# Kernel optimization log

Measured on AMD Instinct MI355X. Metric: run time of the kernel, lower is better.

The kernel has to match this reference:

```python
import jax, jax.numpy as jnp
import numpy as np

DIM = 1024
ATT_DIM = 1024
NUM_HEADS = 16
HEAD_DIM = ATT_DIM // NUM_HEADS


def setup_inputs() -> dict:
    key = jax.random.key(0)
    ks = jax.random.split(key, 13)
    s = lambda fan_in: 1.0 / np.sqrt(fan_in)
    bsz, n = 8, 1024
    x = jax.random.normal(ks[0], (bsz, n, DIM), dtype=jnp.float32)
    # Linear weights stored as [in, out] (apply via x @ W + b)
    Wq = jax.random.uniform(ks[1], (DIM, ATT_DIM), minval=-s(DIM), maxval=s(DIM))
    bq = jax.random.uniform(ks[2], (ATT_DIM,), minval=-s(DIM), maxval=s(DIM))
    Wk = jax.random.uniform(ks[3], (DIM, ATT_DIM), minval=-s(DIM), maxval=s(DIM))
    bk = jax.random.uniform(ks[4], (ATT_DIM,), minval=-s(DIM), maxval=s(DIM))
    Wv = jax.random.uniform(ks[5], (DIM, ATT_DIM), minval=-s(DIM), maxval=s(DIM))
    bv = jax.random.uniform(ks[6], (ATT_DIM,), minval=-s(DIM), maxval=s(DIM))
    Win = jax.random.uniform(ks[7], (DIM, HEAD_DIM), minval=-s(DIM), maxval=s(DIM))
    bin_ = jax.random.uniform(ks[8], (HEAD_DIM,), minval=-s(DIM), maxval=s(DIM))
    d_in1 = HEAD_DIM * (NUM_HEADS + 1)
    W1 = jax.random.uniform(ks[9], (d_in1, 2 * DIM), minval=-s(d_in1), maxval=s(d_in1))
    b1 = jax.random.uniform(ks[10], (2 * DIM,), minval=-s(d_in1), maxval=s(d_in1))
    W2 = jax.random.uniform(ks[11], (2 * DIM, DIM), minval=-s(2 * DIM), maxval=s(2 * DIM))
    b2 = jax.random.uniform(ks[12], (DIM,), minval=-s(2 * DIM), maxval=s(2 * DIM))
    return {"x": x, "Wq": Wq, "bq": bq, "Wk": Wk, "bk": bk, "Wv": Wv, "bv": bv,
            "Win": Win, "bin_": bin_, "W1": W1, "b1": b1, "W2": W2, "b2": b2}


def reference(x, Wq, bq, Wk, bk, Wv, bv, Win, bin_, W1, b1, W2, b2):
    bsz, n, _ = x.shape
    scaling = HEAD_DIM ** (-0.5)
    # [b, n, h, d]
    q = (x @ Wq + bq).reshape(bsz, n, NUM_HEADS, HEAD_DIM) * scaling
    k = (x @ Wk + bk).reshape(bsz, n, NUM_HEADS, HEAD_DIM)
    v = (x @ Wv + bv).reshape(bsz, n, NUM_HEADS, HEAD_DIM)
    # scores [b, h, n, n]
    score = jnp.einsum('bihd,bjhd->bhij', q, k)
    diag = jnp.eye(n, dtype=bool)  # self positions masked with -inf
    score = jnp.where(diag[None, None], -jnp.inf, score)
    attn = jax.nn.softmax(score, axis=-1)
    out = jnp.einsum('bhij,bjhd->bihd', attn, v).reshape(bsz, n, NUM_HEADS * HEAD_DIM)
    in_ = (x @ Win + bin_)  # [b, n, head_dim]
    out = jnp.concatenate([out, in_], axis=-1)
    h = jax.nn.relu(out @ W1 + b1)
    return h @ W2 + b2
```

## Files before the change

### kernel.cpp

```cpp
#include <hip/hip_runtime.h>

typedef __bf16 bf16;
typedef __attribute__((ext_vector_type(8))) __bf16 bf16x8;
typedef __attribute__((ext_vector_type(4))) __bf16 bf16x4;
typedef __attribute__((ext_vector_type(4))) short short4_t;
typedef __attribute__((ext_vector_type(4))) float floatx4;

typedef const void __attribute__((address_space(1)))* gas1p;
typedef void __attribute__((address_space(3)))* las3p;

#define LOG2E 1.44269504088896340736f

static constexpr int D_MODEL = 1024;
static constexpr int N_HEADS = 16;
static constexpr int HDIM    = 64;
static constexpr int BSZ     = 8;
static constexpr int SEQ     = 1024;
static constexpr int ROWS    = BSZ * SEQ;
static constexpr int FF_IN   = 1088;
static constexpr int FF_HID  = 2048;
static constexpr int QKV_LD  = 3072;

__device__ __forceinline__ floatx4 mfma_bf16(bf16x8 a, bf16x8 b, floatx4 c) {
  return __builtin_amdgcn_mfma_f32_16x16x32_bf16(a, b, c, 0, 0, 0);
}

__device__ __forceinline__ floatx4 mfma16(bf16x4 a, bf16x4 b, floatx4 c) {
#if __has_builtin(__builtin_amdgcn_mfma_f32_16x16x16_bf16)
  return __builtin_amdgcn_mfma_f32_16x16x16_bf16(a, b, c, 0, 0, 0);
#else
  return __builtin_amdgcn_mfma_f32_16x16x16bf16_1k(
      __builtin_bit_cast(short4_t, a), __builtin_bit_cast(short4_t, b), c, 0, 0, 0);
#endif
}

__device__ __forceinline__ float flex_load(const void* src, size_t idx, int isbf) {
  return isbf ? (float)((const bf16*)src)[idx] : ((const float*)src)[idx];
}

__global__ void detect_kernel(const unsigned* __restrict__ w, int* __restrict__ flag) {
  __shared__ int cnt;
  if (threadIdx.x == 0) cnt = 0;
  __syncthreads();
  int hits = 0;
  for (int i = threadIdx.x; i < 4096; i += 256) {
    const unsigned v = w[(size_t)i * 997 + 13];
    const unsigned b = (v >> 8) & 0x7F;
    hits += (b >= 0x3B && b <= 0x41) ? 1 : 0;
  }
  atomicAdd(&cnt, hits);
  __syncthreads();
  if (threadIdx.x == 0) *flag = (cnt > 2048) ? 1 : 0;
}

__global__ __launch_bounds__(256)
void x_to_bf16_kernel(const void* __restrict__ src, bf16* __restrict__ dst,
                      const int* __restrict__ flag) {
  const int isbf = *flag;
  const size_t i = ((size_t)blockIdx.x * 256 + threadIdx.x) * 8;
  bf16x8 o;
  if (isbf) {
    o = *reinterpret_cast<const bf16x8*>((const bf16*)src + i);
  } else {
    const float4 f0 = *reinterpret_cast<const float4*>((const float*)src + i);
    const float4 f1 = *reinterpret_cast<const float4*>((const float*)src + i + 4);
    o[0] = (bf16)f0.x; o[1] = (bf16)f0.y; o[2] = (bf16)f0.z; o[3] = (bf16)f0.w;
    o[4] = (bf16)f1.x; o[5] = (bf16)f1.y; o[6] = (bf16)f1.z; o[7] = (bf16)f1.w;
  }
  *reinterpret_cast<bf16x8*>(dst + i) = o;
}

__global__ __launch_bounds__(256)
void bias_all_kernel(const void* bq, const void* bk, const void* bv,
                     const void* bin, const void* b1, const void* b2,
                     float* __restrict__ dst, const int* __restrict__ flag) {
  const int isbf = *flag;
  const int i = blockIdx.x * 256 + threadIdx.x;
  if (i < 1024)      dst[i] = flex_load(bq, i, isbf) * 0.125f;
  else if (i < 2048) dst[i] = flex_load(bk, i - 1024, isbf);
  else if (i < 3072) dst[i] = flex_load(bv, i - 2048, isbf);
  else if (i < 3136) dst[i] = flex_load(bin, i - 3072, isbf);
  else if (i < 5184) dst[i] = flex_load(b1, i - 3136, isbf);
  else if (i < 6208) dst[i] = flex_load(b2, i - 5184, isbf);
}

struct TransJobs {
  const void* src[6];
  bf16* dst[6];
  int R[6], C[6];
  int tiles_x[6];
  int tile_base[7];
  float scale[6];
};

__global__ __launch_bounds__(256)
void transpose_all_kernel(TransJobs J, const int* __restrict__ flag) {
  __shared__ float tile[32][33];
  const int isbf = *flag;
  const int bid = blockIdx.x;
  int j = 0;
#pragma unroll
  for (int t = 1; t < 6; t++) j += (bid >= J.tile_base[t]) ? 1 : 0;
  const int t = bid - J.tile_base[j];
  const int c0 = (t % J.tiles_x[j]) * 32, r0 = (t / J.tiles_x[j]) * 32;
  const void* src = J.src[j];
  bf16* dst = J.dst[j];
  const int R = J.R[j], C = J.C[j];
  const float scale = J.scale[j];
  const int tx = threadIdx.x & 31, ty = threadIdx.x >> 5;
  for (int i = ty; i < 32; i += 8)
    tile[i][tx] = flex_load(src, (size_t)(r0 + i) * C + (c0 + tx), isbf);
  __syncthreads();
  for (int i = ty; i < 32; i += 8)
    dst[(size_t)(c0 + i) * R + (r0 + tx)] = (bf16)(tile[tx][i] * scale);
}

__global__ __launch_bounds__(256)
void transpose_v_kernel(const bf16* __restrict__ v, bf16* __restrict__ vt) {
  __shared__ float tile[32][33];
  const int bh = blockIdx.z, b = bh >> 4, h = bh & 15;
  const int s0 = blockIdx.x * 32, d0 = blockIdx.y * 32;
  const int tx = threadIdx.x & 31, ty = threadIdx.x >> 5;
  const bf16* src = v + (size_t)b * SEQ * QKV_LD + 2048 + h * HDIM;
  bf16* dst = vt + (size_t)bh * HDIM * SEQ;
  for (int i = ty; i < 32; i += 8)
    tile[i][tx] = (float)src[(size_t)(s0 + i) * QKV_LD + d0 + tx];
  __syncthreads();
  for (int i = ty; i < 32; i += 8)
    dst[(size_t)(d0 + i) * SEQ + s0 + tx] = (bf16)tile[tx][i];
}

template <int BN, bool DO_RELU, bool OUT_FLEX>
__global__ __launch_bounds__(256)
void gemm_bt(const bf16* __restrict__ A, const bf16* __restrict__ BT,
             const float* __restrict__ bias,
             void* __restrict__ Cv, int N, int K, int ldc,
             bf16* __restrict__ C2, int ldc2, int nsplit, int nvalid,
             const int* __restrict__ flag) {
  constexpr int BM = 128, BK = 64;
  constexpr int TCN = BN / 32;
  constexpr int ACH = (BM * BK) / (256 * 8);
  constexpr int BCH = (BN * BK) / (256 * 8);
  __shared__ bf16 As[BM * BK];
  __shared__ bf16 Bs[BN * BK];
  const int tid = threadIdx.x;
  const int wave = tid >> 6, lane = tid & 63;
  const int quad = lane >> 4, lo = lane & 15;
  const int wm = wave >> 1, wn = wave & 1;
  const int m0 = blockIdx.x * BM;
  const int n0 = blockIdx.y * BN;

  floatx4 acc[4][TCN];
#pragma unroll
  for (int i = 0; i < 4; i++)
#pragma unroll
    for (int j = 0; j < TCN; j++) acc[i][j] = floatx4{0.f, 0.f, 0.f, 0.f};

  for (int kb = 0; kb < K; kb += BK) {
#pragma unroll
    for (int u = 0; u < ACH; u++) {
      const int c = u * 256 + tid;
      const int row = c >> 3, col = c & 7;
      const int gcol = col ^ (row & 7);
      const bf16* g = A + (size_t)(m0 + row) * K + kb + gcol * 8;
      __builtin_amdgcn_global_load_lds((gas1p)g, (las3p)(As + c * 8), 16, 0, 0);
    }
#pragma unroll
    for (int u = 0; u < BCH; u++) {
      const int c = u * 256 + tid;
      const int row = c >> 3, col = c & 7;
      const int gcol = col ^ (row & 7);
      const bf16* g = BT + (size_t)(n0 + row) * K + kb + gcol * 8;
      __builtin_amdgcn_global_load_lds((gas1p)g, (las3p)(Bs + c * 8), 16, 0, 0);
    }
    __syncthreads();
#pragma unroll
    for (int kk = 0; kk < 2; kk++) {
      bf16x8 af[4], bfr[TCN];
#pragma unroll
      for (int tr = 0; tr < 4; tr++) {
        const int row = wm * 64 + tr * 16 + lo;
        const int cc = (kk * 4 + quad) ^ (lo & 7);
        af[tr] = *reinterpret_cast<const bf16x8*>(As + row * BK + cc * 8);
      }
#pragma unroll
      for (int tc = 0; tc < TCN; tc++) {
        const int row = wn * (BN / 2) + tc * 16 + lo;
        const int cc = (kk * 4 + quad) ^ (lo & 7);
        bfr[tc] = *reinterpret_cast<const bf16x8*>(Bs + row * BK + cc * 8);
      }
#pragma unroll
      for (int tr = 0; tr < 4; tr++)
#pragma unroll
        for (int tc = 0; tc < TCN; tc++)
          acc[tr][tc] = mfma_bf16(af[tr], bfr[tc], acc[tr][tc]);
    }
    __syncthreads();
  }

  const int isbf = OUT_FLEX ? *flag : 1;
#pragma unroll
  for (int tc = 0; tc < TCN; tc++) {
    const int col = n0 + wn * (BN / 2) + tc * 16 + lo;
    const float bval = bias[col];
    if (col < nsplit) {
#pragma unroll
      for (int tr = 0; tr < 4; tr++) {
        const int rbase = m0 + wm * 64 + tr * 16 + quad * 4;
#pragma unroll
        for (int r = 0; r < 4; r++) {
          float v = acc[tr][tc][r] + bval;
          if (DO_RELU) v = fmaxf(v, 0.f);
          const size_t idx = (size_t)(rbase + r) * ldc + col;
          if (!OUT_FLEX || isbf) ((bf16*)Cv)[idx] = (bf16)v;
          else                   ((float*)Cv)[idx] = v;
        }
      }
    } else if (col < nvalid) {
#pragma unroll
      for (int tr = 0; tr < 4; tr++) {
        const int rbase = m0 + wm * 64 + tr * 16 + quad * 4;
#pragma unroll
        for (int r = 0; r < 4; r++) {
          float v = acc[tr][tc][r] + bval;
          if (DO_RELU) v = fmaxf(v, 0.f);
          C2[(size_t)(rbase + r) * ldc2 + (col - nsplit)] = (bf16)v;
        }
      }
    }
  }
}

__global__ __launch_bounds__(256)
void attn_kernel(const bf16* __restrict__ QKV, const bf16* __restrict__ Vt,
                 bf16* __restrict__ Cc) {
  __shared__ bf16 Ks[64 * 64];
  __shared__ bf16 Vs[64 * 64];
  const int bid = blockIdx.x;
  const int xcd = bid & 7, g = bid >> 3;
  const int ib = g & 7, bh = (g >> 3) * 8 + xcd;
  const int b = bh >> 4, h = bh & 15;
  const int i0 = ib * 128;
  const int tid = threadIdx.x, wave = tid >> 6, lane = tid & 63;
  const int quad = lane >> 4, lo = lane & 15;
  const int iw = i0 + wave * 32;
  const bf16* qptr = QKV + (size_t)b * SEQ * QKV_LD + h * HDIM;
  const bf16* kptr = QKV + (size_t)b * SEQ * QKV_LD + 1024 + h * HDIM;
  const bf16* vptr = Vt + (size_t)bh * HDIM * SEQ;

  bf16x8 qf[2][2];
#pragma unroll
  for (int it = 0; it < 2; it++)
#pragma unroll
    for (int kf = 0; kf < 2; kf++)
      qf[it][kf] = *reinterpret_cast<const bf16x8*>(
          qptr + (size_t)(iw + it * 16 + lo) * QKV_LD + kf * 32 + quad * 8);

  floatx4 oacc[2][4];
  float lrow[2] = {0.f, 0.f};
#pragma unroll
  for (int it = 0; it < 2; it++)
#pragma unroll
    for (int dt = 0; dt < 4; dt++) oacc[it][dt] = floatx4{0.f, 0.f, 0.f, 0.f};

  for (int jb = 0; jb < SEQ / 64; jb++) {
    const int j0 = jb * 64;
#pragma unroll
    for (int u = 0; u < 2; u++) {
      const int c = u * 256 + tid;
      const int row = c >> 3, col = c & 7;
      const int gcol = col ^ (row & 7);
      __builtin_amdgcn_global_load_lds(
          (gas1p)(kptr + (size_t)(j0 + row) * QKV_LD + gcol * 8),
          (las3p)(Ks + c * 8), 16, 0, 0);
      __builtin_amdgcn_global_load_lds(
          (gas1p)(vptr + (size_t)row * SEQ + j0 + gcol * 8),
          (las3p)(Vs + c * 8), 16, 0, 0);
    }
    __syncthreads();

    floatx4 sacc[2][4];
#pragma unroll
    for (int it = 0; it < 2; it++)
#pragma unroll
      for (int mt = 0; mt < 4; mt++) sacc[it][mt] = floatx4{0.f, 0.f, 0.f, 0.f};
#pragma unroll
    for (int mt = 0; mt < 4; mt++) {
      const int r = mt * 16 + lo;
      const int cc0 = quad ^ (lo & 7);
      const int cc1 = (4 + quad) ^ (lo & 7);
      const bf16x8 k0 = *reinterpret_cast<const bf16x8*>(Ks + r * 64 + cc0 * 8);
      const bf16x8 k1 = *reinterpret_cast<const bf16x8*>(Ks + r * 64 + cc1 * 8);
#pragma unroll
      for (int it = 0; it < 2; it++) {
        sacc[it][mt] = mfma_bf16(k0, qf[it][0], sacc[it][mt]);
        sacc[it][mt] = mfma_bf16(k1, qf[it][1], sacc[it][mt]);
      }
    }

    if (j0 == (iw & ~63)) {
#pragma unroll
      for (int it = 0; it < 2; it++) {
        const int ig = iw + it * 16 + lo;
#pragma unroll
        for (int mt = 0; mt < 4; mt++)
#pragma unroll
          for (int r = 0; r < 4; r++)
            if (j0 + mt * 16 + quad * 4 + r == ig) sacc[it][mt][r] = -1e30f;
      }
    }

    bf16x4 pfrag[2][4];
#pragma unroll
    for (int it = 0; it < 2; it++) {
      float s = 0.f;
#pragma unroll
      for (int mt = 0; mt < 4; mt++) {
        bf16x4 pk;
#pragma unroll
        for (int r = 0; r < 4; r++) {
          const float p = exp2f(sacc[it][mt][r] * LOG2E);
          s += p;
          pk[r] = (bf16)p;
        }
        pfrag[it][mt] = pk;
      }
      s += __shfl_xor(s, 16);
      s += __shfl_xor(s, 32);
      lrow[it] += s;
    }

#pragma unroll
    for (int dt = 0; dt < 4; dt++) {
      const int r = dt * 16 + lo;
#pragma unroll
      for (int kt = 0; kt < 4; kt++) {
        const int gch = kt * 2 + (quad >> 1);
        const int cc = gch ^ (lo & 7);
        const bf16x4 vf = *reinterpret_cast<const bf16x4*>(
            Vs + r * 64 + cc * 8 + (quad & 1) * 4);
#pragma unroll
        for (int it = 0; it < 2; it++)
          oacc[it][dt] = mfma16(vf, pfrag[it][kt], oacc[it][dt]);
      }
    }
    __syncthreads();
  }

#pragma unroll
  for (int it = 0; it < 2; it++) {
    const int ig = iw + it * 16 + lo;
    const float inv = 1.0f / lrow[it];
    bf16* cb = Cc + ((size_t)b * SEQ + ig) * FF_IN + h * HDIM;
#pragma unroll
    for (int dt = 0; dt < 4; dt++) {
      bf16x4 o;
#pragma unroll
      for (int r = 0; r < 4; r++) o[r] = (bf16)(oacc[it][dt][r] * inv);
      *reinterpret_cast<bf16x4*>(cb + dt * 16 + quad * 4) = o;
    }
  }
}

extern "C" void kernel_launch(void* const* d_in, const int* in_sizes, int n_in,
                              void* d_out, int out_size, void* d_ws, size_t ws_size,
                              hipStream_t stream) {
  (void)in_sizes; (void)n_in; (void)out_size; (void)ws_size;
  const void* x   = d_in[0];
  const void* Wq  = d_in[1];
  const void* bq  = d_in[2];
  const void* Wk  = d_in[3];
  const void* bk  = d_in[4];
  const void* Wv  = d_in[5];
  const void* bv  = d_in[6];
  const void* Win = d_in[7];
  const void* bin = d_in[8];
  const void* W1  = d_in[9];
  const void* b1  = d_in[10];
  const void* W2  = d_in[11];
  const void* b2  = d_in[12];

  size_t off = 0;
  char* wsb = (char*)d_ws;
  auto alloc = [&](size_t bytes) {
    void* p = (void*)(wsb + off);
    off += (bytes + 255) & ~(size_t)255;
    return p;
  };
  int*   flag  = (int*)alloc(4);
  bf16*  xbf   = (bf16*)alloc((size_t)ROWS * D_MODEL * 2);
  bf16*  WqkvT = (bf16*)alloc((size_t)3200 * 1024 * 2);
  bf16*  W1T   = (bf16*)alloc((size_t)FF_HID * FF_IN * 2);
  bf16*  W2T   = (bf16*)alloc((size_t)D_MODEL * FF_HID * 2);
  float* biasf = (float*)alloc(6208 * 4);
  bf16*  qkv   = (bf16*)alloc((size_t)ROWS * QKV_LD * 2);
  bf16*  vtb   = (bf16*)alloc((size_t)ROWS * D_MODEL * 2);
  bf16*  cbuf  = (bf16*)alloc((size_t)ROWS * FF_IN * 2);
  bf16*  hbuf  = (bf16*)alloc((size_t)ROWS * FF_HID * 2);
  float* b1f   = biasf + 3136;
  float* b2f   = biasf + 5184;

  const dim3 blk(256);
  detect_kernel<<<1, blk, 0, stream>>>((const unsigned*)x, flag);

  x_to_bf16_kernel<<<(ROWS * D_MODEL) / 2048, blk, 0, stream>>>(x, xbf, flag);
  bias_all_kernel<<<25, blk, 0, stream>>>(bq, bk, bv, bin, b1, b2, biasf, flag);

  TransJobs J;
  J.src[0] = Wq;  J.dst[0] = WqkvT;                        J.R[0] = 1024; J.C[0] = 1024; J.scale[0] = 0.125f;
  J.src[1] = Wk;  J.dst[1] = WqkvT + (size_t)1024 * 1024;  J.R[1] = 1024; J.C[1] = 1024; J.scale[1] = 1.0f;
  J.src[2] = Wv;  J.dst[2] = WqkvT + (size_t)2048 * 1024;  J.R[2] = 1024; J.C[2] = 1024; J.scale[2] = 1.0f;
  J.src[3] = Win; J.dst[3] = WqkvT + (size_t)3072 * 1024;  J.R[3] = 1024; J.C[3] = 64;   J.scale[3] = 1.0f;
  J.src[4] = W1;  J.dst[4] = W1T;                          J.R[4] = 1088; J.C[4] = 2048; J.scale[4] = 1.0f;
  J.src[5] = W2;  J.dst[5] = W2T;                          J.R[5] = 2048; J.C[5] = 1024; J.scale[5] = 1.0f;
  int base = 0;
  for (int j = 0; j < 6; j++) {
    J.tiles_x[j] = J.C[j] / 32;
    J.tile_base[j] = base;
    base += (J.R[j] / 32) * (J.C[j] / 32);
  }
  J.tile_base[6] = base;
  transpose_all_kernel<<<base, blk, 0, stream>>>(J, flag);

  gemm_bt<128, false, false><<<dim3(ROWS / 128, 25), blk, 0, stream>>>(
      xbf, WqkvT, biasf, qkv, 3200, 1024, QKV_LD,
      cbuf + 1024, FF_IN, 3072, 3136, nullptr);

  transpose_v_kernel<<<dim3(SEQ / 32, HDIM / 32, BSZ * N_HEADS), blk, 0, stream>>>(qkv, vtb);

  attn_kernel<<<dim3(1024), blk, 0, stream>>>(qkv, vtb, cbuf);

  gemm_bt<128, true, false><<<dim3(ROWS / 128, FF_HID / 128), blk, 0, stream>>>(
      cbuf, W1T, b1f, hbuf, FF_HID, FF_IN, FF_HID,
      nullptr, 0, FF_HID, FF_HID, nullptr);
  gemm_bt<128, false, true><<<dim3(ROWS / 128, D_MODEL / 128), blk, 0, stream>>>(
      hbuf, W2T, b2f, d_out, D_MODEL, FF_HID, D_MODEL,
      nullptr, 0, D_MODEL, D_MODEL, flag);
}
```

Baseline: 398.3 us.

## Double-buffer K/V tiles in attention and fold log2e into Q scaling

The attention kernel now keeps two LDS buffers for K and V and issues the next tile's global-to-LDS loads before computing on the current one, so load latency overlaps MFMA work. It also folds the log2e factor into the Q weight and bias scaling, which removes a multiply per score before exp2, splits the row-sum into two accumulators, and raises wave priority around the MFMA blocks. The cost is doubled LDS per block (32KB), which may reduce occupancy, and the correctness of the loop depends on the single barrier per iteration also covering the prefetch.

Result: slower. 407.6 us (+2.3%).

```diff
diff --git a/kernel.cpp b/kernel.cpp
--- a/kernel.cpp
+++ b/kernel.cpp
@@ -76,7 +76,7 @@
                      float* __restrict__ dst, const int* __restrict__ flag) {
   const int isbf = *flag;
   const int i = blockIdx.x * 256 + threadIdx.x;
-  if (i < 1024)      dst[i] = flex_load(bq, i, isbf) * 0.125f;
+  if (i < 1024)      dst[i] = flex_load(bq, i, isbf) * (0.125f * LOG2E);
   else if (i < 2048) dst[i] = flex_load(bk, i - 1024, isbf);
   else if (i < 3072) dst[i] = flex_load(bv, i - 2048, isbf);
   else if (i < 3136) dst[i] = flex_load(bin, i - 3072, isbf);
@@ -234,8 +234,8 @@
 __global__ __launch_bounds__(256)
 void attn_kernel(const bf16* __restrict__ QKV, const bf16* __restrict__ Vt,
                  bf16* __restrict__ Cc) {
-  __shared__ bf16 Ks[64 * 64];
-  __shared__ bf16 Vs[64 * 64];
+  __shared__ bf16 Ks[2][64 * 64];
+  __shared__ bf16 Vs[2][64 * 64];
   const int bid = blockIdx.x;
   const int xcd = bid & 7, g = bid >> 3;
   const int ib = g & 7, bh = (g >> 3) * 8 + xcd;
@@ -248,6 +248,10 @@
   const bf16* kptr = QKV + (size_t)b * SEQ * QKV_LD + 1024 + h * HDIM;
   const bf16* vptr = Vt + (size_t)bh * HDIM * SEQ;
 
+  const int c0 = tid, c1 = 256 + tid;
+  const int row0 = c0 >> 3, gcol0 = (c0 & 7) ^ (row0 & 7);
+  const int row1 = c1 >> 3, gcol1 = (c1 & 7) ^ (row1 & 7);
+
   bf16x8 qf[2][2];
 #pragma unroll
   for (int it = 0; it < 2; it++)
@@ -263,40 +267,65 @@
 #pragma unroll
     for (int dt = 0; dt < 4; dt++) oacc[it][dt] = floatx4{0.f, 0.f, 0.f, 0.f};
 
+  {
+    __builtin_amdgcn_global_load_lds(
+        (gas1p)(kptr + (size_t)row0 * QKV_LD + gcol0 * 8),
+        (las3p)(Ks[0] + c0 * 8), 16, 0, 0);
+    __builtin_amdgcn_global_load_lds(
+        (gas1p)(vptr + (size_t)row0 * SEQ + gcol0 * 8),
+        (las3p)(Vs[0] + c0 * 8), 16, 0, 0);
+    __builtin_amdgcn_global_load_lds(
+        (gas1p)(kptr + (size_t)row1 * QKV_LD + gcol1 * 8),
+        (las3p)(Ks[0] + c1 * 8), 16, 0, 0);
+    __builtin_amdgcn_global_load_lds(
+        (gas1p)(vptr + (size_t)row1 * SEQ + gcol1 * 8),
+        (las3p)(Vs[0] + c1 * 8), 16, 0, 0);
+  }
+  __syncthreads();
+
   for (int jb = 0; jb < SEQ / 64; jb++) {
     const int j0 = jb * 64;
-#pragma unroll
-    for (int u = 0; u < 2; u++) {
-      const int c = u * 256 + tid;
-      const int row = c >> 3, col = c & 7;
-      const int gcol = col ^ (row & 7);
+    const int cur = jb & 1;
+
+    if (jb + 1 < SEQ / 64) {
+      const int jn = j0 + 64;
       __builtin_amdgcn_global_load_lds(
-          (gas1p)(kptr + (size_t)(j0 + row) * QKV_LD + gcol * 8),
-          (las3p)(Ks + c * 8), 16, 0, 0);
+          (gas1p)(kptr + (size_t)(jn + row0) * QKV_LD + gcol0 * 8),
+          (las3p)(Ks[cur ^ 1] + c0 * 8), 16, 0, 0);
       __builtin_amdgcn_global_load_lds(
-          (gas1p)(vptr + (size_t)row * SEQ + j0 + gcol * 8),
-          (las3p)(Vs + c * 8), 16, 0, 0);
-    }
-    __syncthreads();
+          (gas1p)(vptr + (size_t)row0 * SEQ + jn + gcol0 * 8),
+          (las3p)(Vs[cur ^ 1] + c0 * 8), 16, 0, 0);
+      __builtin_amdgcn_global_load_lds(
+          (gas1p)(kptr + (size_t)(jn + row1) * QKV_LD + gcol1 * 8),
+          (las3p)(Ks[cur ^ 1] + c1 * 8), 16, 0, 0);
+      __builtin_amdgcn_global_load_lds(
+          (gas1p)(vptr + (size_t)row1 * SEQ + jn + gcol1 * 8),
+          (las3p)(Vs[cur ^ 1] + c1 * 8), 16, 0, 0);
+    }
+
+    const bf16* Kc = Ks[cur];
+    const bf16* Vc = Vs[cur];
 
     floatx4 sacc[2][4];
 #pragma unroll
     for (int it = 0; it < 2; it++)
 #pragma unroll
       for (int mt = 0; mt < 4; mt++) sacc[it][mt] = floatx4{0.f, 0.f, 0.f, 0.f};
+    __builtin_amdgcn_s_setprio(1);
 #pragma unroll
     for (int mt = 0; mt < 4; mt++) {
       const int r = mt * 16 + lo;
       const int cc0 = quad ^ (lo & 7);
       const int cc1 = (4 + quad) ^ (lo & 7);
-      const bf16x8 k0 = *reinterpret_cast<const bf16x8*>(Ks + r * 64 + cc0 * 8);
-      const bf16x8 k1 = *reinterpret_cast<const bf16x8*>(Ks + r * 64 + cc1 * 8);
+      const bf16x8 k0 = *reinterpret_cast<const bf16x8*>(Kc + r * 64 + cc0 * 8);
+      const bf16x8 k1 = *reinterpret_cast<const bf16x8*>(Kc + r * 64 + cc1 * 8);
 #pragma unroll
       for (int it = 0; it < 2; it++) {
         sacc[it][mt] = mfma_bf16(k0, qf[it][0], sacc[it][mt]);
         sacc[it][mt] = mfma_bf16(k1, qf[it][1], sacc[it][mt]);
       }
     }
+    __builtin_amdgcn_s_setprio(0);
 
     if (j0 == (iw & ~63)) {
 #pragma unroll
@@ -313,23 +342,25 @@
     bf16x4 pfrag[2][4];
 #pragma unroll
     for (int it = 0; it < 2; it++) {
-      float s = 0.f;
+      float s0 = 0.f, s1 = 0.f;
 #pragma unroll
       for (int mt = 0; mt < 4; mt++) {
         bf16x4 pk;
 #pragma unroll
         for (int r = 0; r < 4; r++) {
-          const float p = exp2f(sacc[it][mt][r] * LOG2E);
-          s += p;
+          const float p = exp2f(sacc[it][mt][r]);
+          if (mt & 1) s1 += p; else s0 += p;
           pk[r] = (bf16)p;
         }
         pfrag[it][mt] = pk;
       }
+      float s = s0 + s1;
       s += __shfl_xor(s, 16);
       s += __shfl_xor(s, 32);
       lrow[it] += s;
     }
 
+    __builtin_amdgcn_s_setprio(1);
 #pragma unroll
     for (int dt = 0; dt < 4; dt++) {
       const int r = dt * 16 + lo;
@@ -338,12 +369,14 @@
         const int gch = kt * 2 + (quad >> 1);
         const int cc = gch ^ (lo & 7);
         const bf16x4 vf = *reinterpret_cast<const bf16x4*>(
-            Vs + r * 64 + cc * 8 + (quad & 1) * 4);
+            Vc + r * 64 + cc * 8 + (quad & 1) * 4);
 #pragma unroll
         for (int it = 0; it < 2; it++)
           oacc[it][dt] = mfma16(vf, pfrag[it][kt], oacc[it][dt]);
       }
     }
+    __builtin_amdgcn_s_setprio(0);
+
     __syncthreads();
   }
 
@@ -407,7 +440,7 @@
   bias_all_kernel<<<25, blk, 0, stream>>>(bq, bk, bv, bin, b1, b2, biasf, flag);
 
   TransJobs J;
-  J.src[0] = Wq;  J.dst[0] = WqkvT;                        J.R[0] = 1024; J.C[0] = 1024; J.scale[0] = 0.125f;
+  J.src[0] = Wq;  J.dst[0] = WqkvT;                        J.R[0] = 1024; J.C[0] = 1024; J.scale[0] = 0.125f * LOG2E;
   J.src[1] = Wk;  J.dst[1] = WqkvT + (size_t)1024 * 1024;  J.R[1] = 1024; J.C[1] = 1024; J.scale[1] = 1.0f;
   J.src[2] = Wv;  J.dst[2] = WqkvT + (size_t)2048 * 1024;  J.R[2] = 1024; J.C[2] = 1024; J.scale[2] = 1.0f;
   J.src[3] = Win; J.dst[3] = WqkvT + (size_t)3072 * 1024;  J.R[3] = 1024; J.C[3] = 64;   J.scale[3] = 1.0f;
```

## Triple-buffer GEMM with 256x128 tiles, fold log2e into Q scaling

Applied to the files above, without the earlier changes.

The GEMM grows to 256x128 tiles run by 512 threads, with a three-stage LDS ring buffer. Async global-to-LDS loads are issued up to three K-steps ahead and tracked with explicit vmcnt waits, which hides global latency behind MFMA work. The attention kernel drops a multiply per score by folding LOG2E into the Q weight and bias scale, raises wave priority around its MFMA sections, and splits the row-sum accumulator in two. The ring buffer uses about 144KB of LDS per block, so only one block fits per CU despite the launch-bounds hint, and the larger tiles halve the grid size.

Measured after the change: 416.7 us. +4.6%, slower.

```diff
diff --git a/kernel.cpp b/kernel.cpp
--- a/kernel.cpp
+++ b/kernel.cpp
@@ -76,7 +76,7 @@
                      float* __restrict__ dst, const int* __restrict__ flag) {
   const int isbf = *flag;
   const int i = blockIdx.x * 256 + threadIdx.x;
-  if (i < 1024)      dst[i] = flex_load(bq, i, isbf) * 0.125f;
+  if (i < 1024)      dst[i] = flex_load(bq, i, isbf) * (0.125f * LOG2E);
   else if (i < 2048) dst[i] = flex_load(bk, i - 1024, isbf);
   else if (i < 3072) dst[i] = flex_load(bv, i - 2048, isbf);
   else if (i < 3136) dst[i] = flex_load(bin, i - 3072, isbf);
@@ -131,24 +131,24 @@
 }
 
 template <int BN, bool DO_RELU, bool OUT_FLEX>
-__global__ __launch_bounds__(256)
+__global__ __launch_bounds__(512, 2)
 void gemm_bt(const bf16* __restrict__ A, const bf16* __restrict__ BT,
              const float* __restrict__ bias,
              void* __restrict__ Cv, int N, int K, int ldc,
              bf16* __restrict__ C2, int ldc2, int nsplit, int nvalid,
              const int* __restrict__ flag) {
-  constexpr int BM = 128, BK = 64;
+  constexpr int BM = 256, BK = 64;
   constexpr int TCN = BN / 32;
-  constexpr int ACH = (BM * BK) / (256 * 8);
-  constexpr int BCH = (BN * BK) / (256 * 8);
-  __shared__ bf16 As[BM * BK];
-  __shared__ bf16 Bs[BN * BK];
+  static_assert(BN == 128, "BN must be 128");
+  __shared__ bf16 As[3][BM * BK];
+  __shared__ bf16 Bs[3][BN * BK];
   const int tid = threadIdx.x;
   const int wave = tid >> 6, lane = tid & 63;
   const int quad = lane >> 4, lo = lane & 15;
   const int wm = wave >> 1, wn = wave & 1;
   const int m0 = blockIdx.x * BM;
   const int n0 = blockIdx.y * BN;
+  const int NT = K / BK;
 
   floatx4 acc[4][TCN];
 #pragma unroll
@@ -156,24 +156,36 @@
 #pragma unroll
     for (int j = 0; j < TCN; j++) acc[i][j] = floatx4{0.f, 0.f, 0.f, 0.f};
 
-  for (int kb = 0; kb < K; kb += BK) {
-#pragma unroll
-    for (int u = 0; u < ACH; u++) {
-      const int c = u * 256 + tid;
-      const int row = c >> 3, col = c & 7;
-      const int gcol = col ^ (row & 7);
-      const bf16* g = A + (size_t)(m0 + row) * K + kb + gcol * 8;
-      __builtin_amdgcn_global_load_lds((gas1p)g, (las3p)(As + c * 8), 16, 0, 0);
-    }
-#pragma unroll
-    for (int u = 0; u < BCH; u++) {
-      const int c = u * 256 + tid;
-      const int row = c >> 3, col = c & 7;
-      const int gcol = col ^ (row & 7);
-      const bf16* g = BT + (size_t)(n0 + row) * K + kb + gcol * 8;
-      __builtin_amdgcn_global_load_lds((gas1p)g, (las3p)(Bs + c * 8), 16, 0, 0);
-    }
-    __syncthreads();
+  auto stage = [&](int t, int cb) {
+    const size_t kb = (size_t)t * BK;
+#pragma unroll
+    for (int u = 0; u < 4; u++) {
+      const int c = u * 512 + tid;
+      const int row = c >> 3;
+      const int gcol = (c & 7) ^ (row & 7);
+      __builtin_amdgcn_global_load_lds(
+          (gas1p)(A + (size_t)(m0 + row) * K + kb + gcol * 8),
+          (las3p)(&As[cb][c * 8]), 16, 0, 0);
+    }
+#pragma unroll
+    for (int u = 0; u < 2; u++) {
+      const int c = u * 512 + tid;
+      const int row = c >> 3;
+      const int gcol = (c & 7) ^ (row & 7);
+      __builtin_amdgcn_global_load_lds(
+          (gas1p)(BT + (size_t)(n0 + row) * K + kb + gcol * 8),
+          (las3p)(&Bs[cb][c * 8]), 16, 0, 0);
+    }
+  };
+
+  stage(0, 0); stage(1, 1); stage(2, 2);
+  asm volatile("s_waitcnt vmcnt(12)" ::: "memory");
+  asm volatile("s_barrier" ::: "memory");
+
+  for (int kt = 0; kt < NT; ++kt) {
+    const int cb = kt % 3;
+    const bf16* Asc = As[cb];
+    const bf16* Bsc = Bs[cb];
 #pragma unroll
     for (int kk = 0; kk < 2; kk++) {
       bf16x8 af[4], bfr[TCN];
@@ -181,13 +193,13 @@
       for (int tr = 0; tr < 4; tr++) {
         const int row = wm * 64 + tr * 16 + lo;
         const int cc = (kk * 4 + quad) ^ (lo & 7);
-        af[tr] = *reinterpret_cast<const bf16x8*>(As + row * BK + cc * 8);
+        af[tr] = *reinterpret_cast<const bf16x8*>(Asc + row * BK + cc * 8);
       }
 #pragma unroll
       for (int tc = 0; tc < TCN; tc++) {
         const int row = wn * (BN / 2) + tc * 16 + lo;
         const int cc = (kk * 4 + quad) ^ (lo & 7);
-        bfr[tc] = *reinterpret_cast<const bf16x8*>(Bs + row * BK + cc * 8);
+        bfr[tc] = *reinterpret_cast<const bf16x8*>(Bsc + row * BK + cc * 8);
       }
 #pragma unroll
       for (int tr = 0; tr < 4; tr++)
@@ -195,7 +207,16 @@
         for (int tc = 0; tc < TCN; tc++)
           acc[tr][tc] = mfma_bf16(af[tr], bfr[tc], acc[tr][tc]);
     }
-    __syncthreads();
+    if (kt + 1 < NT) {
+      asm volatile("s_waitcnt lgkmcnt(0)" ::: "memory");
+      asm volatile("s_barrier" ::: "memory");
+      if (kt + 3 < NT) stage(kt + 3, cb);
+      const int ahead = ((kt + 3 < NT) ? (kt + 3) : (NT - 1)) - (kt + 1);
+      if (ahead >= 2)      asm volatile("s_waitcnt vmcnt(12)" ::: "memory");
+      else if (ahead == 1) asm volatile("s_waitcnt vmcnt(6)" ::: "memory");
+      else                 asm volatile("s_waitcnt vmcnt(0)" ::: "memory");
+      asm volatile("s_barrier" ::: "memory");
+    }
   }
 
   const int isbf = OUT_FLEX ? *flag : 1;
@@ -284,6 +305,7 @@
     for (int it = 0; it < 2; it++)
 #pragma unroll
       for (int mt = 0; mt < 4; mt++) sacc[it][mt] = floatx4{0.f, 0.f, 0.f, 0.f};
+    __builtin_amdgcn_s_setprio(1);
 #pragma unroll
     for (int mt = 0; mt < 4; mt++) {
       const int r = mt * 16 + lo;
@@ -297,6 +319,7 @@
         sacc[it][mt] = mfma_bf16(k1, qf[it][1], sacc[it][mt]);
       }
     }
+    __builtin_amdgcn_s_setprio(0);
 
     if (j0 == (iw & ~63)) {
 #pragma unroll
@@ -313,23 +336,25 @@
     bf16x4 pfrag[2][4];
 #pragma unroll
     for (int it = 0; it < 2; it++) {
-      float s = 0.f;
+      float s0 = 0.f, s1 = 0.f;
 #pragma unroll
       for (int mt = 0; mt < 4; mt++) {
         bf16x4 pk;
 #pragma unroll
         for (int r = 0; r < 4; r++) {
-          const float p = exp2f(sacc[it][mt][r] * LOG2E);
-          s += p;
+          const float p = exp2f(sacc[it][mt][r]);
+          if (mt & 1) s1 += p; else s0 += p;
           pk[r] = (bf16)p;
         }
         pfrag[it][mt] = pk;
       }
+      float s = s0 + s1;
       s += __shfl_xor(s, 16);
       s += __shfl_xor(s, 32);
       lrow[it] += s;
     }
 
+    __builtin_amdgcn_s_setprio(1);
 #pragma unroll
     for (int dt = 0; dt < 4; dt++) {
       const int r = dt * 16 + lo;
@@ -344,6 +369,7 @@
           oacc[it][dt] = mfma16(vf, pfrag[it][kt], oacc[it][dt]);
       }
     }
+    __builtin_amdgcn_s_setprio(0);
     __syncthreads();
   }
 
@@ -401,13 +427,14 @@
   float* b2f   = biasf + 5184;
 
   const dim3 blk(256);
+  const dim3 blk512(512);
   detect_kernel<<<1, blk, 0, stream>>>((const unsigned*)x, flag);
 
   x_to_bf16_kernel<<<(ROWS * D_MODEL) / 2048, blk, 0, stream>>>(x, xbf, flag);
   bias_all_kernel<<<25, blk, 0, stream>>>(bq, bk, bv, bin, b1, b2, biasf, flag);
 
   TransJobs J;
-  J.src[0] = Wq;  J.dst[0] = WqkvT;                        J.R[0] = 1024; J.C[0] = 1024; J.scale[0] = 0.125f;
+  J.src[0] = Wq;  J.dst[0] = WqkvT;                        J.R[0] = 1024; J.C[0] = 1024; J.scale[0] = 0.125f * LOG2E;
   J.src[1] = Wk;  J.dst[1] = WqkvT + (size_t)1024 * 1024;  J.R[1] = 1024; J.C[1] = 1024; J.scale[1] = 1.0f;
   J.src[2] = Wv;  J.dst[2] = WqkvT + (size_t)2048 * 1024;  J.R[2] = 1024; J.C[2] = 1024; J.scale[2] = 1.0f;
   J.src[3] = Win; J.dst[3] = WqkvT + (size_t)3072 * 1024;  J.R[3] = 1024; J.C[3] = 64;   J.scale[3] = 1.0f;
@@ -422,7 +449,7 @@
   J.tile_base[6] = base;
   transpose_all_kernel<<<base, blk, 0, stream>>>(J, flag);
 
-  gemm_bt<128, false, false><<<dim3(ROWS / 128, 25), blk, 0, stream>>>(
+  gemm_bt<128, false, false><<<dim3(ROWS / 256, 25), blk512, 0, stream>>>(
       xbf, WqkvT, biasf, qkv, 3200, 1024, QKV_LD,
       cbuf + 1024, FF_IN, 3072, 3136, nullptr);
 
@@ -430,10 +457,10 @@
 
   attn_kernel<<<dim3(1024), blk, 0, stream>>>(qkv, vtb, cbuf);
 
-  gemm_bt<128, true, false><<<dim3(ROWS / 128, FF_HID / 128), blk, 0, stream>>>(
+  gemm_bt<128, true, false><<<dim3(ROWS / 256, FF_HID / 128), blk512, 0, stream>>>(
       cbuf, W1T, b1f, hbuf, FF_HID, FF_IN, FF_HID,
       nullptr, 0, FF_HID, FF_HID, nullptr);
-  gemm_bt<128, false, true><<<dim3(ROWS / 128, D_MODEL / 128), blk, 0, stream>>>(
+  gemm_bt<128, false, true><<<dim3(ROWS / 256, D_MODEL / 128), blk512, 0, stream>>>(
       hbuf, W2T, b2f, d_out, D_MODEL, FF_HID, D_MODEL,
       nullptr, 0, D_MODEL, D_MODEL, flag);
 }
```
